# Kernel tuning notes

Hardware: AMD Instinct MI355X
Metric: run time of the kernel (lower is better)

## Reference

```python
import jax, jax.numpy as jnp
import numpy as np
import math

N_WIRES = 8
DIM = 2 ** N_WIRES  # 256

# Pauli-Z sign table: wire 0 is the most-significant axis of the statevector.
_idx = np.arange(DIM)
_SIGNS = np.stack([1.0 - 2.0 * ((_idx >> (N_WIRES - 1 - w)) & 1) for w in range(N_WIRES)], axis=1).astype(np.float32)  # [256, 8]


def _cnot(state, c, t):
    # state: [N, 2, 2, ..., 2]; flip target axis where control bit == 1
    s0, s1 = jnp.split(state, 2, axis=1 + c)
    s1 = jnp.flip(s1, axis=1 + t)
    return jnp.concatenate([s0, s1], axis=1 + c)


def _quantum_heads(x, theta):
    """Simulate the QLayer circuit. x: [N, 8] -> PauliZ expectations [N, 8].

    Circuit: RX(x_i) then RX(theta_i) on wire i (commute -> RX(x_i+theta_i)),
    CNOT chain (0,1)...(6,7),(7,0), MeasureAll(PauliZ).
    """
    phi = 0.5 * (x + theta)  # RX half-angle
    c = jnp.cos(phi)
    s = jnp.sin(phi)
    # RX(a)|0> = cos(a/2)|0> - i sin(a/2)|1>
    amps = jax.lax.complex(jnp.stack([c, jnp.zeros_like(c)], axis=-1),
                           jnp.stack([jnp.zeros_like(s), -s], axis=-1))  # [N, 8, 2] complex64
    # Product state as rank-8 tensor [N, 2, ..., 2]
    state = amps[:, 0]
    for w in range(1, N_WIRES):
        state = state[..., None] * amps[:, w].reshape((-1,) + (1,) * w + (2,))
    # Entangling CNOT ring
    for w in range(N_WIRES - 1):
        state = _cnot(state, w, w + 1)
    state = _cnot(state, N_WIRES - 1, 0)
    probs = jnp.abs(state.reshape(-1, DIM)) ** 2  # [N, 256]
    return probs @ jnp.asarray(_SIGNS)  # [N, 8]


def setup_inputs() -> dict:
    key = jax.random.key(0)
    k1, k2, k3, k4 = jax.random.split(key, 4)
    B, S, E = 32, 512, 64
    return {
        "x": jax.random.normal(k1, (B, S, E), dtype=jnp.float32),
        "theta": jax.random.normal(k2, (N_WIRES,), dtype=jnp.float32),
        "W": jax.random.normal(k3, (E, E), dtype=jnp.float32) * 0.05,
        "b": jax.random.normal(k4, (E,), dtype=jnp.float32) * 0.05,
    }


def reference(x, theta, W, b):
    B, S, E = x.shape
    H = E // N_WIRES  # num_heads
    # q = k = v: same deterministic quantum projection applied to the same x.
    z = _quantum_heads(x.reshape(B * S * H, N_WIRES), theta).reshape(B, S, H, N_WIRES)
    scale = 1.0 / math.sqrt(E // H)
    # NOTE: matmul over last dims -> attention across heads within each token.
    scores = jnp.einsum('bshd,bstd->bsht', z, z) * scale  # [B, S, H, H]
    attn = jax.nn.softmax(scores, axis=-1)
    out = jnp.einsum('bsht,bstd->bshd', attn, z).reshape(B, S, E)
    return out @ W.T + b
```

## Files before the change

### kernel.cpp

```cpp
#include <hip/hip_runtime.h>


#define TOK_PER_BLK 16

typedef __attribute__((ext_vector_type(8))) short short8;
typedef __attribute__((ext_vector_type(4))) float f32x4;

__device__ inline unsigned short f2bf(float f) {
    unsigned u = __float_as_uint(f);
    u += 0x7FFF + ((u >> 16) & 1);
    return (unsigned short)(u >> 16);
}

__device__ inline short8 pack_bf16x8(float4 a, float4 b) {
    short8 r;
    r[0] = (short)f2bf(a.x); r[1] = (short)f2bf(a.y);
    r[2] = (short)f2bf(a.z); r[3] = (short)f2bf(a.w);
    r[4] = (short)f2bf(b.x); r[5] = (short)f2bf(b.y);
    r[6] = (short)f2bf(b.z); r[7] = (short)f2bf(b.w);
    return r;
}

__global__ __launch_bounds__(256, 4)
void mhaq_fused5(const float* __restrict__ x,
                 const float* __restrict__ theta,
                 const float* __restrict__ W,
                 const float* __restrict__ bias,
                 float* __restrict__ out,
                 int n_tokens)
{
    __shared__ __align__(16) float          zs[TOK_PER_BLK * 68];
    __shared__ __align__(16) unsigned short os[TOK_PER_BLK * 72];

    const int tid  = threadIdx.x;
    const int tl   = tid >> 4;
    const int s    = tid & 15;
    const int h    = s >> 1;
    const int half = s & 1;
    const int blockbase = blockIdx.x * TOK_PER_BLK;
    const int token = blockbase + tl;
    const bool zrole = (s < 8);

    float4 xa = make_float4(0.f, 0.f, 0.f, 0.f);
    float4 xb = make_float4(0.f, 0.f, 0.f, 0.f);
    if (zrole && token < n_tokens) {
        const float4* __restrict__ xp =
            reinterpret_cast<const float4*>(x) + (size_t)token * 16 + s * 2;
        xa = xp[0]; xb = xp[1];
    }

    const int lane = tid & 63;
    const int wave = tid >> 6;
    const int lr   = lane & 15;
    const int lg   = lane >> 4;
    const int j    = wave * 16 + lr;
    float4 wf[2][2];
    float  bj = bias[j];
    {
        const float4* __restrict__ Wv = reinterpret_cast<const float4*>(W);
        #pragma unroll
        for (int kt = 0; kt < 2; ++kt) {
            int fidx = (j * 64 + kt * 32 + lg * 8) >> 2;
            wf[kt][0] = Wv[fidx];
            wf[kt][1] = Wv[fidx + 1];
        }
    }

    if (zrole) {
        float c0 = __cosf(xa.x + theta[0]);
        float c1 = __cosf(xa.y + theta[1]);
        float c2 = __cosf(xa.z + theta[2]);
        float c3 = __cosf(xa.w + theta[3]);
        float c4 = __cosf(xb.x + theta[4]);
        float c5 = __cosf(xb.y + theta[5]);
        float c6 = __cosf(xb.z + theta[6]);
        float c7 = __cosf(xb.w + theta[7]);
        float p1 = c0 * c1;
        float p2 = p1 * c2;
        float p3 = p2 * c3;
        float p4 = p3 * c4;
        float p5 = p4 * c5;
        float p6 = p5 * c6;
        float p7 = p6 * c7;
        float s6 = c6 * c7;
        float s5 = c5 * s6;
        float s4 = c4 * s5;
        float s3 = c3 * s4;
        float s2 = c2 * s3;
        float s1 = c1 * s2;
        float4* z4 = reinterpret_cast<float4*>(zs + tl * 68 + s * 8);
        z4[0] = make_float4(s1, p1, p2, p3);
        z4[1] = make_float4(p4, p5, p6, p7);
    }
    __syncthreads();

    {
        const float* zrow = zs + tl * 68;
        float zh[8];
        *reinterpret_cast<float4*>(&zh[0]) =
            *reinterpret_cast<const float4*>(&zrow[h * 8]);
        *reinterpret_cast<float4*>(&zh[4]) =
            *reinterpret_cast<const float4*>(&zrow[h * 8 + 4]);

        float zt[32];
        #pragma unroll
        for (int i = 0; i < 8; ++i)
            *reinterpret_cast<float4*>(&zt[i * 4]) =
                *reinterpret_cast<const float4*>(&zrow[half * 32 + i * 4]);

        const float scale = 0.35355339059327373f;
        float e[4];
        float psum = 0.f;
        #pragma unroll
        for (int tt = 0; tt < 4; ++tt) {
            float sd = 0.f;
            #pragma unroll
            for (int d = 0; d < 8; ++d)
                sd = fmaf(zh[d], zt[tt * 8 + d], sd);
            e[tt] = __expf(sd * scale);
            psum += e[tt];
        }
        float tot = psum + __shfl_xor(psum, 1, 64);
        float inv = 1.0f / tot;

        float ep[4];
        #pragma unroll
        for (int tt = 0; tt < 4; ++tt)
            ep[tt] = __shfl_xor(e[tt], 1, 64);

        float ef[8];
        #pragma unroll
        for (int tt = 0; tt < 4; ++tt) {
            ef[tt]     = half ? ep[tt] : e[tt];
            ef[4 + tt] = half ? e[tt]  : ep[tt];
        }

        float zc[32];
        #pragma unroll
        for (int t = 0; t < 8; ++t)
            *reinterpret_cast<float4*>(&zc[t * 4]) =
                *reinterpret_cast<const float4*>(&zrow[t * 8 + half * 4]);

        unsigned short oh[4];
        #pragma unroll
        for (int dd = 0; dd < 4; ++dd) {
            float acc = 0.f;
            #pragma unroll
            for (int t = 0; t < 8; ++t)
                acc = fmaf(ef[t], zc[t * 4 + dd], acc);
            oh[dd] = f2bf(acc * inv);
        }
        *reinterpret_cast<ushort4*>(&os[tl * 72 + h * 8 + half * 4]) =
            make_ushort4(oh[0], oh[1], oh[2], oh[3]);
    }
    __syncthreads();

    {
        short8 afrag[2];
        #pragma unroll
        for (int kt = 0; kt < 2; ++kt)
            afrag[kt] = *reinterpret_cast<const short8*>(
                &os[lr * 72 + kt * 32 + lg * 8]);

        f32x4 acc = {bj, bj, bj, bj};
        #pragma unroll
        for (int kt = 0; kt < 2; ++kt) {
            short8 bfrag = pack_bf16x8(wf[kt][0], wf[kt][1]);
            acc = __builtin_amdgcn_mfma_f32_16x16x32_bf16(
                afrag[kt], bfrag, acc, 0, 0, 0);
        }
        #pragma unroll
        for (int r = 0; r < 4; ++r) {
            int trow = blockbase + lg * 4 + r;
            if (trow < n_tokens)
                out[(size_t)trow * 64 + j] = acc[r];
        }
    }
}

extern "C" void kernel_launch(void* const* d_in, const int* in_sizes, int n_in,
                              void* d_out, int out_size, void* d_ws, size_t ws_size,
                              hipStream_t stream)
{
    const float* x     = (const float*)d_in[0];
    const float* theta = (const float*)d_in[1];
    const float* W     = (const float*)d_in[2];
    const float* b     = (const float*)d_in[3];
    float* out         = (float*)d_out;

    const int n_tokens = in_sizes[0] / 64;
    const int blocks   = (n_tokens + TOK_PER_BLK - 1) / TOK_PER_BLK;
    mhaq_fused5<<<blocks, 256, 0, stream>>>(x, theta, W, b, out, n_tokens);
}
```

Baseline: 9.764 us.

## Process four token tiles per block with register prefetch of next tile

Each block now loops over four 16-token tiles instead of handling one. The next tile's x values are prefetched into registers while the current tile is computed, and the W fragments are loaded and packed to bf16 only once per block. The aim is to amortize the W/bias loads and bf16 packing and to hide global load latency. In exchange the grid shrinks fourfold, to roughly one block per CU on this input, and each tile still runs serialized behind two block barriers, which may reduce latency hiding.

New measurement: 10.98 us. 12.4% more time.

```diff
diff --git a/kernel.cpp b/kernel.cpp
--- a/kernel.cpp
+++ b/kernel.cpp
@@ -1,7 +1,8 @@
 #include <hip/hip_runtime.h>
 
 
-#define TOK_PER_BLK 16
+#define TILE_TOK 16
+#define NTILES 4
 
 typedef __attribute__((ext_vector_type(8))) short short8;
 typedef __attribute__((ext_vector_type(4))) float f32x4;
@@ -22,38 +23,38 @@
 }
 
 __global__ __launch_bounds__(256, 4)
-void mhaq_fused5(const float* __restrict__ x,
+void mhaq_fused7(const float* __restrict__ x,
                  const float* __restrict__ theta,
                  const float* __restrict__ W,
                  const float* __restrict__ bias,
                  float* __restrict__ out,
                  int n_tokens)
 {
-    __shared__ __align__(16) float          zs[TOK_PER_BLK * 68];
-    __shared__ __align__(16) unsigned short os[TOK_PER_BLK * 72];
+    __shared__ __align__(16) float          zs[TILE_TOK * 68];
+    __shared__ __align__(16) unsigned short os[TILE_TOK * 72];
 
     const int tid  = threadIdx.x;
     const int tl   = tid >> 4;
     const int s    = tid & 15;
     const int h    = s >> 1;
     const int half = s & 1;
-    const int blockbase = blockIdx.x * TOK_PER_BLK;
-    const int token = blockbase + tl;
+    const int blockbase = blockIdx.x * (TILE_TOK * NTILES);
     const bool zrole = (s < 8);
-
-    float4 xa = make_float4(0.f, 0.f, 0.f, 0.f);
-    float4 xb = make_float4(0.f, 0.f, 0.f, 0.f);
-    if (zrole && token < n_tokens) {
-        const float4* __restrict__ xp =
-            reinterpret_cast<const float4*>(x) + (size_t)token * 16 + s * 2;
-        xa = xp[0]; xb = xp[1];
-    }
 
     const int lane = tid & 63;
     const int wave = tid >> 6;
     const int lr   = lane & 15;
     const int lg   = lane >> 4;
     const int j    = wave * 16 + lr;
+
+    const float4* __restrict__ xp4 = reinterpret_cast<const float4*>(x);
+    float4 xa = make_float4(0.f, 0.f, 0.f, 0.f);
+    float4 xb = make_float4(0.f, 0.f, 0.f, 0.f);
+    if (zrole && blockbase + tl < n_tokens) {
+        const float4* p = xp4 + (size_t)(blockbase + tl) * 16 + s * 2;
+        xa = p[0]; xb = p[1];
+    }
+
     float4 wf[2][2];
     float  bj = bias[j];
     {
@@ -66,115 +67,129 @@
         }
     }
 
-    if (zrole) {
-        float c0 = __cosf(xa.x + theta[0]);
-        float c1 = __cosf(xa.y + theta[1]);
-        float c2 = __cosf(xa.z + theta[2]);
-        float c3 = __cosf(xa.w + theta[3]);
-        float c4 = __cosf(xb.x + theta[4]);
-        float c5 = __cosf(xb.y + theta[5]);
-        float c6 = __cosf(xb.z + theta[6]);
-        float c7 = __cosf(xb.w + theta[7]);
-        float p1 = c0 * c1;
-        float p2 = p1 * c2;
-        float p3 = p2 * c3;
-        float p4 = p3 * c4;
-        float p5 = p4 * c5;
-        float p6 = p5 * c6;
-        float p7 = p6 * c7;
-        float s6 = c6 * c7;
-        float s5 = c5 * s6;
-        float s4 = c4 * s5;
-        float s3 = c3 * s4;
-        float s2 = c2 * s3;
-        float s1 = c1 * s2;
-        float4* z4 = reinterpret_cast<float4*>(zs + tl * 68 + s * 8);
-        z4[0] = make_float4(s1, p1, p2, p3);
-        z4[1] = make_float4(p4, p5, p6, p7);
-    }
-    __syncthreads();
-
-    {
-        const float* zrow = zs + tl * 68;
-        float zh[8];
-        *reinterpret_cast<float4*>(&zh[0]) =
-            *reinterpret_cast<const float4*>(&zrow[h * 8]);
-        *reinterpret_cast<float4*>(&zh[4]) =
-            *reinterpret_cast<const float4*>(&zrow[h * 8 + 4]);
-
-        float zt[32];
-        #pragma unroll
-        for (int i = 0; i < 8; ++i)
-            *reinterpret_cast<float4*>(&zt[i * 4]) =
-                *reinterpret_cast<const float4*>(&zrow[half * 32 + i * 4]);
-
-        const float scale = 0.35355339059327373f;
-        float e[4];
-        float psum = 0.f;
-        #pragma unroll
-        for (int tt = 0; tt < 4; ++tt) {
-            float sd = 0.f;
-            #pragma unroll
-            for (int d = 0; d < 8; ++d)
-                sd = fmaf(zh[d], zt[tt * 8 + d], sd);
-            e[tt] = __expf(sd * scale);
-            psum += e[tt];
-        }
-        float tot = psum + __shfl_xor(psum, 1, 64);
-        float inv = 1.0f / tot;
-
-        float ep[4];
-        #pragma unroll
-        for (int tt = 0; tt < 4; ++tt)
-            ep[tt] = __shfl_xor(e[tt], 1, 64);
-
-        float ef[8];
-        #pragma unroll
-        for (int tt = 0; tt < 4; ++tt) {
-            ef[tt]     = half ? ep[tt] : e[tt];
-            ef[4 + tt] = half ? e[tt]  : ep[tt];
-        }
-
-        float zc[32];
-        #pragma unroll
-        for (int t = 0; t < 8; ++t)
-            *reinterpret_cast<float4*>(&zc[t * 4]) =
-                *reinterpret_cast<const float4*>(&zrow[t * 8 + half * 4]);
-
-        unsigned short oh[4];
-        #pragma unroll
-        for (int dd = 0; dd < 4; ++dd) {
-            float acc = 0.f;
-            #pragma unroll
-            for (int t = 0; t < 8; ++t)
-                acc = fmaf(ef[t], zc[t * 4 + dd], acc);
-            oh[dd] = f2bf(acc * inv);
-        }
-        *reinterpret_cast<ushort4*>(&os[tl * 72 + h * 8 + half * 4]) =
-            make_ushort4(oh[0], oh[1], oh[2], oh[3]);
-    }
-    __syncthreads();
-
-    {
-        short8 afrag[2];
-        #pragma unroll
-        for (int kt = 0; kt < 2; ++kt)
-            afrag[kt] = *reinterpret_cast<const short8*>(
-                &os[lr * 72 + kt * 32 + lg * 8]);
-
-        f32x4 acc = {bj, bj, bj, bj};
-        #pragma unroll
-        for (int kt = 0; kt < 2; ++kt) {
-            short8 bfrag = pack_bf16x8(wf[kt][0], wf[kt][1]);
-            acc = __builtin_amdgcn_mfma_f32_16x16x32_bf16(
-                afrag[kt], bfrag, acc, 0, 0, 0);
-        }
-        #pragma unroll
-        for (int r = 0; r < 4; ++r) {
-            int trow = blockbase + lg * 4 + r;
-            if (trow < n_tokens)
-                out[(size_t)trow * 64 + j] = acc[r];
-        }
+    short8 bfrag0, bfrag1;
+
+    #pragma unroll
+    for (int t = 0; t < NTILES; ++t) {
+        const int tilebase = blockbase + t * TILE_TOK;
+
+        float4 xa_n = make_float4(0.f, 0.f, 0.f, 0.f);
+        float4 xb_n = make_float4(0.f, 0.f, 0.f, 0.f);
+        if (t + 1 < NTILES && zrole && tilebase + TILE_TOK + tl < n_tokens) {
+            const float4* p = xp4 + (size_t)(tilebase + TILE_TOK + tl) * 16 + s * 2;
+            xa_n = p[0]; xb_n = p[1];
+        }
+
+        if (zrole) {
+            float c0 = __cosf(xa.x + theta[0]);
+            float c1 = __cosf(xa.y + theta[1]);
+            float c2 = __cosf(xa.z + theta[2]);
+            float c3 = __cosf(xa.w + theta[3]);
+            float c4 = __cosf(xb.x + theta[4]);
+            float c5 = __cosf(xb.y + theta[5]);
+            float c6 = __cosf(xb.z + theta[6]);
+            float c7 = __cosf(xb.w + theta[7]);
+            float p1 = c0 * c1;
+            float p2 = p1 * c2;
+            float p3 = p2 * c3;
+            float p4 = p3 * c4;
+            float p5 = p4 * c5;
+            float p6 = p5 * c6;
+            float p7 = p6 * c7;
+            float s6 = c6 * c7;
+            float s5 = c5 * s6;
+            float s4 = c4 * s5;
+            float s3 = c3 * s4;
+            float s2 = c2 * s3;
+            float s1 = c1 * s2;
+            float4* z4 = reinterpret_cast<float4*>(zs + tl * 68 + s * 8);
+            z4[0] = make_float4(s1, p1, p2, p3);
+            z4[1] = make_float4(p4, p5, p6, p7);
+        }
+        __syncthreads();
+
+        {
+            const float* zrow = zs + tl * 68;
+            float zh[8];
+            *reinterpret_cast<float4*>(&zh[0]) =
+                *reinterpret_cast<const float4*>(&zrow[h * 8]);
+            *reinterpret_cast<float4*>(&zh[4]) =
+                *reinterpret_cast<const float4*>(&zrow[h * 8 + 4]);
+
+            float zt[32];
+            #pragma unroll
+            for (int i = 0; i < 8; ++i)
+                *reinterpret_cast<float4*>(&zt[i * 4]) =
+                    *reinterpret_cast<const float4*>(&zrow[half * 32 + i * 4]);
+
+            const float scale = 0.35355339059327373f;
+            float e[4];
+            float psum = 0.f;
+            #pragma unroll
+            for (int tt = 0; tt < 4; ++tt) {
+                float sd = 0.f;
+                #pragma unroll
+                for (int d = 0; d < 8; ++d)
+                    sd = fmaf(zh[d], zt[tt * 8 + d], sd);
+                e[tt] = __expf(sd * scale);
+                psum += e[tt];
+            }
+            float tot = psum + __shfl_xor(psum, 1, 64);
+            float inv = 1.0f / tot;
+
+            float ep[4];
+            #pragma unroll
+            for (int tt = 0; tt < 4; ++tt)
+                ep[tt] = __shfl_xor(e[tt], 1, 64);
+
+            float ef[8];
+            #pragma unroll
+            for (int tt = 0; tt < 4; ++tt) {
+                ef[tt]     = half ? ep[tt] : e[tt];
+                ef[4 + tt] = half ? e[tt]  : ep[tt];
+            }
+
+            float zc[32];
+            #pragma unroll
+            for (int tt = 0; tt < 8; ++tt)
+                *reinterpret_cast<float4*>(&zc[tt * 4]) =
+                    *reinterpret_cast<const float4*>(&zrow[tt * 8 + half * 4]);
+
+            unsigned short oh[4];
+            #pragma unroll
+            for (int dd = 0; dd < 4; ++dd) {
+                float acc = 0.f;
+                #pragma unroll
+                for (int tt = 0; tt < 8; ++tt)
+                    acc = fmaf(ef[tt], zc[tt * 4 + dd], acc);
+                oh[dd] = f2bf(acc * inv);
+            }
+            *reinterpret_cast<ushort4*>(&os[tl * 72 + h * 8 + half * 4]) =
+                make_ushort4(oh[0], oh[1], oh[2], oh[3]);
+        }
+        __syncthreads();
+
+        {
+            if (t == 0) {
+                bfrag0 = pack_bf16x8(wf[0][0], wf[0][1]);
+                bfrag1 = pack_bf16x8(wf[1][0], wf[1][1]);
+            }
+            short8 afrag0 = *reinterpret_cast<const short8*>(&os[lr * 72 + lg * 8]);
+            short8 afrag1 = *reinterpret_cast<const short8*>(&os[lr * 72 + 32 + lg * 8]);
+
+            f32x4 acc = {bj, bj, bj, bj};
+            acc = __builtin_amdgcn_mfma_f32_16x16x32_bf16(afrag0, bfrag0, acc, 0, 0, 0);
+            acc = __builtin_amdgcn_mfma_f32_16x16x32_bf16(afrag1, bfrag1, acc, 0, 0, 0);
+
+            #pragma unroll
+            for (int r = 0; r < 4; ++r) {
+                int trow = tilebase + lg * 4 + r;
+                if (trow < n_tokens)
+                    out[(size_t)trow * 64 + j] = acc[r];
+            }
+        }
+
+        xa = xa_n; xb = xb_n;
     }
 }
 
@@ -188,7 +203,8 @@
     const float* b     = (const float*)d_in[3];
     float* out         = (float*)d_out;
 
-    const int n_tokens = in_sizes[0] / 64;
-    const int blocks   = (n_tokens + TOK_PER_BLK - 1) / TOK_PER_BLK;
-    mhaq_fused5<<<blocks, 256, 0, stream>>>(x, theta, W, b, out, n_tokens);
-}
+    const int n_tokens  = in_sizes[0] / 64;
+    const int tok_blk   = TILE_TOK * NTILES;
+    const int blocks    = (n_tokens + tok_blk - 1) / tok_blk;
+    mhaq_fused7<<<blocks, 256, 0, stream>>>(x, theta, W, b, out, n_tokens);
+}
```
